# Kernel tuning notes

Measured on AMD Instinct MI355X. Metric: run time of the kernel, lower is better.

The kernel has to match this reference:

```python
import jax, jax.numpy as jnp
import numpy as np

LAMBDA_S = 1.0   # options['lambda_s']
NITER = 100      # options['iter_ihs']

_HS_FILTER = jnp.array([[1/12, 1/6, 1/12],
                        [1/6,  0.0, 1/6 ],
                        [1/12, 1/6, 1/12]], dtype=jnp.float32)


def _smooth(f):
    # f: [n, h, w] -> 3x3 Horn-Schunck weighted average, zero padding (== torch conv2d padding=1)
    k = _HS_FILTER.reshape(1, 1, 3, 3)  # [out_c, in_c, kh, kw]
    return jax.lax.conv_general_dilated(f[:, None], k, window_strides=(1, 1), padding='SAME')[:, 0]


def setup_inputs() -> dict:
    key = jax.random.key(0)
    k1, k2 = jax.random.split(key)
    n, h, w = 8, 256, 256
    x = jax.random.normal(k1, (n, 3, h, w), dtype=jnp.float32)            # [I_t, I_x, I_y]
    old_estimate = jax.random.normal(k2, (n, 2, h, w), dtype=jnp.float32)  # warm-start (u, v)
    return {"x": x, "old_estimate": old_estimate}


def reference(x, old_estimate):
    # x: [n,3,h,w]; old_estimate: [n,2,h,w]
    I_t, I_x, I_y = x[:, 0], x[:, 1], x[:, 2]
    denom = LAMBDA_S ** 2 + I_x ** 2 + I_y ** 2  # iteration-invariant
    u0, v0 = old_estimate[:, 0], old_estimate[:, 1]  # warm_ihs=True

    def step(carry, _):
        u, v = carry
        u_bar = _smooth(u)
        v_bar = _smooth(v)
        der = (I_x * u_bar + I_y * v_bar + I_t) / denom
        return (u_bar - I_x * der, v_bar - I_y * der), None

    (u, v), _ = jax.lax.scan(step, (u0, v0), None, length=NITER)
    return jnp.stack((u, v), axis=1)  # [n,2,h,w]
```

## Files before the change

### kernel.cpp

```cpp
#include <hip/hip_runtime.h>

typedef unsigned long long ull;

#define HH 256
#define WW 256
#define PLANE (HH*WW)
#define TILE_R 32
#define TILE_C 64
#define TT 8
#define ER (TILE_R + 2*TT)
#define EC (TILE_C + 2*TT)
#define NCP (EC/2)
#define NRG 16
#define RPT (ER/NRG)
#define NTHR 640
#define STRIDE 164
#define LSZ (4 + ER*STRIDE + 4)

#define RING_OFS (2u*1024u*1024u)
#define FLAG_OFS (4u*1024u*1024u)
#define RIMG (HH*(WW/2)*4)
#define NBLK 256

__device__ __forceinline__ void hs_step(
    const float* __restrict__ rbuf, float* __restrict__ wbuf,
    int fb, int rm, int r0, int rN,
    float4* __restrict__ Mreg,
    const float2* __restrict__ ca, const float2* __restrict__ cb,
    const float2* __restrict__ cc, const float2* __restrict__ cd,
    const float2* __restrict__ ce)
{
    const float* qb = rbuf + fb;

    float2 L[RPT+2], R[RPT+2];
    const float* p0 = qb + STRIDE*rm;
    const float* pN = qb + STRIDE*rN;
    L[0] = *(const float2*)(p0 - 2);  R[0] = *(const float2*)(p0 + 4);
    #pragma unroll
    for (int j = 0; j < RPT; ++j) {
        const float* pr = qb + STRIDE*(r0 + j);
        L[j+1] = *(const float2*)(pr - 2);
        R[j+1] = *(const float2*)(pr + 4);
    }
    L[RPT+1] = *(const float2*)(pN - 2);  R[RPT+1] = *(const float2*)(pN + 4);
    float4 Mb0 = *(const float4*)(p0);
    float4 MbN = *(const float4*)(pN);

    float2 hu[RPT+2], hv[RPT+2];
    hu[0] = make_float2(fmaf(2.f,Mb0.x,L[0].x)+Mb0.z, fmaf(2.f,Mb0.z,Mb0.x)+R[0].x);
    hv[0] = make_float2(fmaf(2.f,Mb0.y,L[0].y)+Mb0.w, fmaf(2.f,Mb0.w,Mb0.y)+R[0].y);
    #pragma unroll
    for (int j = 0; j < RPT; ++j) {
        float4 Mc = Mreg[j];
        hu[j+1] = make_float2(fmaf(2.f,Mc.x,L[j+1].x)+Mc.z, fmaf(2.f,Mc.z,Mc.x)+R[j+1].x);
        hv[j+1] = make_float2(fmaf(2.f,Mc.y,L[j+1].y)+Mc.w, fmaf(2.f,Mc.w,Mc.y)+R[j+1].y);
    }
    hu[RPT+1] = make_float2(fmaf(2.f,MbN.x,L[RPT+1].x)+MbN.z, fmaf(2.f,MbN.z,MbN.x)+R[RPT+1].x);
    hv[RPT+1] = make_float2(fmaf(2.f,MbN.y,L[RPT+1].y)+MbN.w, fmaf(2.f,MbN.w,MbN.y)+R[RPT+1].y);

    #pragma unroll
    for (int j = 0; j < RPT; ++j) {
        float4 Mc = Mreg[j];
        float tux = fmaf(-4.f, Mc.x, fmaf(2.f, hu[j+1].x, hu[j].x) + hu[j+2].x);
        float tuy = fmaf(-4.f, Mc.z, fmaf(2.f, hu[j+1].y, hu[j].y) + hu[j+2].y);
        float tvx = fmaf(-4.f, Mc.y, fmaf(2.f, hv[j+1].x, hv[j].x) + hv[j+2].x);
        float tvy = fmaf(-4.f, Mc.w, fmaf(2.f, hv[j+1].y, hv[j].y) + hv[j+2].y);
        float2 un, vn;
        un.x = fmaf(ca[j].x, tux, -fmaf(cb[j].x, tvx, cc[j].x));
        un.y = fmaf(ca[j].y, tuy, -fmaf(cb[j].y, tvy, cc[j].y));
        vn.x = fmaf(cd[j].x, tvx, -fmaf(cb[j].x, tux, ce[j].x));
        vn.y = fmaf(cd[j].y, tvy, -fmaf(cb[j].y, tuy, ce[j].y));
        float4 nv = make_float4(un.x, vn.x, un.y, vn.y);
        *(float4*)(wbuf + STRIDE*(r0 + j) + fb) = nv;
        Mreg[j] = nv;
    }
}

__global__ __launch_bounds__(NTHR, 2)
void hs_mega(const float* __restrict__ x,
             const float* __restrict__ est,
             float* __restrict__ out,
             float* __restrict__ ws)
{
    __shared__ __align__(16) float s0[LSZ];
    __shared__ __align__(16) float s1[LSZ];

    const int img = blockIdx.x, cs = blockIdx.y, rb = blockIdx.z;
    const int tid = threadIdx.x;
    const int er0 = rb*TILE_R - TT;
    const int ec0 = cs*TILE_C - TT;
    const int blin = (img*4 + cs)*8 + rb;
    unsigned* flags = (unsigned*)(ws + FLAG_OFS);

    int nb = -1;
    if (tid < 8) {
        int t = (tid < 4) ? tid : tid + 1;
        int dr = t/3 - 1, dc = t%3 - 1;
        int nrb = rb + dr, ncs = cs + dc;
        if (nrb >= 0 && nrb < 8 && ncs >= 0 && ncs < 4)
            nb = (img*4 + ncs)*8 + nrb;
    }

    const int cp = tid % NCP;
    const int rg = tid / NCP;
    const int r0 = rg * RPT;
    const int fb = 4 + 4*cp;
    const int rm = (r0 == 0) ? 0 : r0 - 1;
    const int rN = (r0 + RPT > ER-1) ? ER-1 : r0+RPT;

    float2 ca[RPT], cb[RPT], cc[RPT], cd[RPT], ce[RPT];
    {
        const float* __restrict__ xit = x + img*3*PLANE;
        const float* __restrict__ xix = xit + PLANE;
        const float* __restrict__ xiy = xix + PLANE;
        #pragma unroll
        for (int i = 0; i < RPT; ++i) {
            int gr = er0 + r0 + i;
            #pragma unroll
            for (int j = 0; j < 2; ++j) {
                int gc = ec0 + 2*cp + j;
                float A=0.f, B=0.f, C=0.f, D=0.f, E=0.f;
                if (gr >= 0 && gr < HH && gc >= 0 && gc < WW) {
                    int q = gr*WW + gc;
                    float it = xit[q], ix = xix[q], iy = xiy[q];
                    float rd = 1.0f / (1.0f + ix*ix + iy*iy);
                    const float s12 = 1.0f/12.0f;
                    A = (1.0f - ix*ix*rd) * s12;
                    B = (ix*iy*rd) * s12;
                    C = ix*it*rd;
                    D = (1.0f - iy*iy*rd) * s12;
                    E = iy*it*rd;
                }
                if (j == 0) { ca[i].x=A; cb[i].x=B; cc[i].x=C; cd[i].x=D; ce[i].x=E; }
                else        { ca[i].y=A; cb[i].y=B; cc[i].y=C; cd[i].y=D; ce[i].y=E; }
            }
        }
    }

    {
        const float* __restrict__ eu = est + img*2*PLANE;
        const float* __restrict__ ev = eu + PLANE;
        for (int k = tid; k < ER*NCP; k += NTHR) {
            int r = k / NCP, c = k - r*NCP;
            int gr = er0 + r, gc = ec0 + 2*c;
            float2 uu = make_float2(0.f,0.f), vv = make_float2(0.f,0.f);
            if (gr >= 0 && gr < HH && gc >= 0 && gc < WW) {
                uu = *(const float2*)(eu + gr*WW + gc);
                vv = *(const float2*)(ev + gr*WW + gc);
            }
            *(float4*)(s0 + 4 + STRIDE*r + 4*c) = make_float4(uu.x, vv.x, uu.y, vv.y);
        }
    }
    __syncthreads();

    float4 Mreg[RPT];
    #pragma unroll
    for (int j = 0; j < RPT; ++j)
        Mreg[j] = *(const float4*)(s0 + STRIDE*(r0 + j) + fb);

    for (int p = 0; p < 13; ++p) {
        if (p < 12) {
            #pragma unroll
            for (int q = 0; q < 4; ++q) {
                hs_step(s0, s1, fb, rm, r0, rN, Mreg, ca, cb, cc, cd, ce);
                __syncthreads();
                hs_step(s1, s0, fb, rm, r0, rN, Mreg, ca, cb, cc, cd, ce);
                __syncthreads();
            }
        } else {
            #pragma unroll
            for (int q = 0; q < 2; ++q) {
                hs_step(s0, s1, fb, rm, r0, rN, Mreg, ca, cb, cc, cd, ce);
                __syncthreads();
                hs_step(s1, s0, fb, rm, r0, rN, Mreg, ca, cb, cc, cd, ce);
                __syncthreads();
            }
        }

        if (p < 12) {
            float* ring = ws + (unsigned)(p & 1) * RING_OFS + img*RIMG;

            for (int k = tid; k < 640; k += NTHR) {
                int m = k; int r, c2;
                if (m < 256)      { r = m >> 5;              c2 = m & 31; }
                else if (m < 512) { r = 24 + ((m-256) >> 5); c2 = (m-256) & 31; }
                else { int mm = m - 512; r = 8 + (mm >> 3); int t = mm & 7; c2 = (t < 4) ? t : 24 + t; }
                const float* sp = s0 + 4 + STRIDE*(r + TT) + 4*(c2 + 4);
                float* gp = ring + ((rb*TILE_R + r)*(WW/2) + cs*(TILE_C/2) + c2)*4;
                __hip_atomic_store((ull*)gp,     *(const ull*)sp,       __ATOMIC_RELAXED, __HIP_MEMORY_SCOPE_AGENT);
                __hip_atomic_store((ull*)gp + 1, *(const ull*)(sp + 2), __ATOMIC_RELAXED, __HIP_MEMORY_SCOPE_AGENT);
            }
            asm volatile("s_waitcnt vmcnt(0)" ::: "memory");
            __syncthreads();
            if (tid == 0)
                __hip_atomic_store(&flags[p*NBLK + blin], 0x5eed0100u + (unsigned)p,
                                   __ATOMIC_RELAXED, __HIP_MEMORY_SCOPE_AGENT);
            asm volatile("" ::: "memory");
            if (tid < 8 && nb >= 0) {
                const unsigned tgt = 0x5eed0100u + (unsigned)p;
                while (__hip_atomic_load(&flags[p*NBLK + nb],
                                         __ATOMIC_RELAXED, __HIP_MEMORY_SCOPE_AGENT) != tgt)
                    __builtin_amdgcn_s_sleep(1);
            }
            __syncthreads();

            for (int k = tid; k < 896; k += NTHR) {
                int m = k; int r, c2;
                if (m < 320)      { r = m / 40;              c2 = m - (m/40)*40; }
                else if (m < 640) { int mm = m-320; r = 40 + mm/40; c2 = mm - (mm/40)*40; }
                else { int mm = m - 640; r = 8 + (mm >> 3); int t = mm & 7; c2 = (t < 4) ? t : 32 + t; }
                int gr = er0 + r, gc2 = cs*(TILE_C/2) - 4 + c2;
                ull v0 = 0, v1 = 0;
                if (gr >= 0 && gr < HH && gc2 >= 0 && gc2 < WW/2) {
                    const float* gp = ring + (gr*(WW/2) + gc2)*4;
                    v0 = __hip_atomic_load((const ull*)gp,     __ATOMIC_RELAXED, __HIP_MEMORY_SCOPE_AGENT);
                    v1 = __hip_atomic_load((const ull*)gp + 1, __ATOMIC_RELAXED, __HIP_MEMORY_SCOPE_AGENT);
                }
                float* sp = s0 + 4 + STRIDE*r + 4*c2;
                *(ull*)sp = v0;
                *(ull*)(sp + 2) = v1;
            }
            __syncthreads();

            #pragma unroll
            for (int j = 0; j < RPT; ++j)
                Mreg[j] = *(const float4*)(s0 + STRIDE*(r0 + j) + fb);
        }
    }

    {
        float* ou = out + img*2*PLANE;
        float* ov = ou + PLANE;
        for (int k = tid; k < 1024; k += NTHR) {
            int r = k >> 5, c2 = k & 31;
            float4 V = *(const float4*)(s0 + 4 + STRIDE*(r + TT) + 4*(c2 + 4));
            int q = (rb*TILE_R + r)*WW + cs*TILE_C + 2*c2;
            *(float2*)(ou + q) = make_float2(V.x, V.z);
            *(float2*)(ov + q) = make_float2(V.y, V.w);
        }
    }
}

extern "C" void kernel_launch(void* const* d_in, const int* in_sizes, int n_in,
                              void* d_out, int out_size, void* d_ws, size_t ws_size,
                              hipStream_t stream) {
    const float* x   = (const float*)d_in[0];
    const float* est = (const float*)d_in[1];
    float* out = (float*)d_out;
    float* ws  = (float*)d_ws;

    dim3 grid(8, WW/TILE_C, HH/TILE_R);
    dim3 blk(NTHR);
    hs_mega<<<grid, blk, 0, stream>>>(x, est, out, ws);
}
```

Measured before the change: 179.3 us.

## Use DPP lane shifts for horizontal stencil neighbors and cut LDS traffic

Each thread now owns six rows instead of three, and each wave maps lanes to column pairs so left and right neighbors come from adjacent lanes through DPP wave shifts rather than LDS loads. Only a thread's first and last rows are written to shared memory on intermediate steps, with a full writeback only before each halo exchange. After an exchange, only halo-region registers are reloaded from LDS. The aim is to remove most LDS reads and writes per step. In exchange, 24 of every 64 lanes sit idle and block size drops to 512 threads. Wrong neighbor values at wave edges are relied on to stay inside the trapezoid halo.

```diff
diff --git a/kernel.cpp b/kernel.cpp
--- a/kernel.cpp
+++ b/kernel.cpp
@@ -11,9 +11,9 @@
 #define ER (TILE_R + 2*TT)
 #define EC (TILE_C + 2*TT)
 #define NCP (EC/2)
-#define NRG 16
+#define NRG 8
 #define RPT (ER/NRG)
-#define NTHR 640
+#define NTHR 512
 #define STRIDE 164
 #define LSZ (4 + ER*STRIDE + 4)
 
@@ -22,41 +22,36 @@
 #define RIMG (HH*(WW/2)*4)
 #define NBLK 256
 
+__device__ __forceinline__ float dpp_prev(float v) {
+    return __int_as_float(__builtin_amdgcn_update_dpp(0, __float_as_int(v), 0x138, 0xF, 0xF, true));
+}
+__device__ __forceinline__ float dpp_next(float v) {
+    return __int_as_float(__builtin_amdgcn_update_dpp(0, __float_as_int(v), 0x130, 0xF, 0xF, true));
+}
+
+__device__ __forceinline__ void hsum(const float4 M, float2& hu, float2& hv) {
+    float Lz = dpp_prev(M.z), Lw = dpp_prev(M.w);
+    float Rx = dpp_next(M.x), Ry = dpp_next(M.y);
+    hu = make_float2(fmaf(2.f, M.x, Lz) + M.z, fmaf(2.f, M.z, M.x) + Rx);
+    hv = make_float2(fmaf(2.f, M.y, Lw) + M.w, fmaf(2.f, M.w, M.y) + Ry);
+}
+
 __device__ __forceinline__ void hs_step(
     const float* __restrict__ rbuf, float* __restrict__ wbuf,
-    int fb, int rm, int r0, int rN,
+    int fb, int rm, int r0, int rN, bool fullwb,
     float4* __restrict__ Mreg,
     const float2* __restrict__ ca, const float2* __restrict__ cb,
     const float2* __restrict__ cc, const float2* __restrict__ cd,
     const float2* __restrict__ ce)
 {
-    const float* qb = rbuf + fb;
-
-    float2 L[RPT+2], R[RPT+2];
-    const float* p0 = qb + STRIDE*rm;
-    const float* pN = qb + STRIDE*rN;
-    L[0] = *(const float2*)(p0 - 2);  R[0] = *(const float2*)(p0 + 4);
+    float4 Mb0 = *(const float4*)(rbuf + STRIDE*rm + fb);
+    float4 MbN = *(const float4*)(rbuf + STRIDE*rN + fb);
+
+    float2 hu[RPT+2], hv[RPT+2];
     #pragma unroll
-    for (int j = 0; j < RPT; ++j) {
-        const float* pr = qb + STRIDE*(r0 + j);
-        L[j+1] = *(const float2*)(pr - 2);
-        R[j+1] = *(const float2*)(pr + 4);
-    }
-    L[RPT+1] = *(const float2*)(pN - 2);  R[RPT+1] = *(const float2*)(pN + 4);
-    float4 Mb0 = *(const float4*)(p0);
-    float4 MbN = *(const float4*)(pN);
-
-    float2 hu[RPT+2], hv[RPT+2];
-    hu[0] = make_float2(fmaf(2.f,Mb0.x,L[0].x)+Mb0.z, fmaf(2.f,Mb0.z,Mb0.x)+R[0].x);
-    hv[0] = make_float2(fmaf(2.f,Mb0.y,L[0].y)+Mb0.w, fmaf(2.f,Mb0.w,Mb0.y)+R[0].y);
-    #pragma unroll
-    for (int j = 0; j < RPT; ++j) {
-        float4 Mc = Mreg[j];
-        hu[j+1] = make_float2(fmaf(2.f,Mc.x,L[j+1].x)+Mc.z, fmaf(2.f,Mc.z,Mc.x)+R[j+1].x);
-        hv[j+1] = make_float2(fmaf(2.f,Mc.y,L[j+1].y)+Mc.w, fmaf(2.f,Mc.w,Mc.y)+R[j+1].y);
-    }
-    hu[RPT+1] = make_float2(fmaf(2.f,MbN.x,L[RPT+1].x)+MbN.z, fmaf(2.f,MbN.z,MbN.x)+R[RPT+1].x);
-    hv[RPT+1] = make_float2(fmaf(2.f,MbN.y,L[RPT+1].y)+MbN.w, fmaf(2.f,MbN.w,MbN.y)+R[RPT+1].y);
+    for (int j = 0; j < RPT; ++j) hsum(Mreg[j], hu[j+1], hv[j+1]);
+    hsum(Mb0, hu[0], hv[0]);
+    hsum(MbN, hu[RPT+1], hv[RPT+1]);
 
     #pragma unroll
     for (int j = 0; j < RPT; ++j) {
@@ -71,8 +66,9 @@
         vn.x = fmaf(cd[j].x, tvx, -fmaf(cb[j].x, tux, ce[j].x));
         vn.y = fmaf(cd[j].y, tvy, -fmaf(cb[j].y, tuy, ce[j].y));
         float4 nv = make_float4(un.x, vn.x, un.y, vn.y);
-        *(float4*)(wbuf + STRIDE*(r0 + j) + fb) = nv;
         Mreg[j] = nv;
+        if (j == 0 || j == RPT-1 || fullwb)
+            *(float4*)(wbuf + STRIDE*(r0 + j) + fb) = nv;
     }
 }
 
@@ -101,15 +97,16 @@
             nb = (img*4 + ncs)*8 + nrb;
     }
 
-    const int cp = tid % NCP;
-    const int rg = tid / NCP;
+    const int cp = tid & 63;
+    const int rg = tid >> 6;
+    const bool act = (cp < NCP);
     const int r0 = rg * RPT;
     const int fb = 4 + 4*cp;
     const int rm = (r0 == 0) ? 0 : r0 - 1;
     const int rN = (r0 + RPT > ER-1) ? ER-1 : r0+RPT;
 
     float2 ca[RPT], cb[RPT], cc[RPT], cd[RPT], ce[RPT];
-    {
+    if (act) {
         const float* __restrict__ xit = x + img*3*PLANE;
         const float* __restrict__ xix = xit + PLANE;
         const float* __restrict__ xiy = xix + PLANE;
@@ -154,25 +151,27 @@
     __syncthreads();
 
     float4 Mreg[RPT];
-    #pragma unroll
-    for (int j = 0; j < RPT; ++j)
-        Mreg[j] = *(const float4*)(s0 + STRIDE*(r0 + j) + fb);
+    if (act) {
+        #pragma unroll
+        for (int j = 0; j < RPT; ++j)
+            Mreg[j] = *(const float4*)(s0 + STRIDE*(r0 + j) + fb);
+    }
 
     for (int p = 0; p < 13; ++p) {
         if (p < 12) {
             #pragma unroll
             for (int q = 0; q < 4; ++q) {
-                hs_step(s0, s1, fb, rm, r0, rN, Mreg, ca, cb, cc, cd, ce);
-                __syncthreads();
-                hs_step(s1, s0, fb, rm, r0, rN, Mreg, ca, cb, cc, cd, ce);
+                if (act) hs_step(s0, s1, fb, rm, r0, rN, false, Mreg, ca, cb, cc, cd, ce);
+                __syncthreads();
+                if (act) hs_step(s1, s0, fb, rm, r0, rN, (q == 3), Mreg, ca, cb, cc, cd, ce);
                 __syncthreads();
             }
         } else {
             #pragma unroll
             for (int q = 0; q < 2; ++q) {
-                hs_step(s0, s1, fb, rm, r0, rN, Mreg, ca, cb, cc, cd, ce);
-                __syncthreads();
-                hs_step(s1, s0, fb, rm, r0, rN, Mreg, ca, cb, cc, cd, ce);
+                if (act) hs_step(s0, s1, fb, rm, r0, rN, false, Mreg, ca, cb, cc, cd, ce);
+                __syncthreads();
+                if (act) hs_step(s1, s0, fb, rm, r0, rN, (q == 1), Mreg, ca, cb, cc, cd, ce);
                 __syncthreads();
             }
         }
@@ -222,9 +221,14 @@
             }
             __syncthreads();
 
-            #pragma unroll
-            for (int j = 0; j < RPT; ++j)
-                Mreg[j] = *(const float4*)(s0 + STRIDE*(r0 + j) + fb);
+            if (act) {
+                #pragma unroll
+                for (int j = 0; j < RPT; ++j) {
+                    int r = r0 + j;
+                    if (r < TT || r >= ER-TT || cp < 4 || cp >= NCP-4)
+                        Mreg[j] = *(const float4*)(s0 + STRIDE*r + fb);
+                }
+            }
         }
     }
 
```

Result: no change. 178.3 us (-0.6%).
